# Kernel optimization log

Measured on AMD Instinct MI355X. Metric: run time of the kernel, lower is better.

Reference implementation:

```python
import jax, jax.numpy as jnp
import numpy as np

EMBED_DIM = 1024
NUM_HEADS = 16
HEAD_DIM = EMBED_DIM // NUM_HEADS


def setup_inputs() -> dict:
    key = jax.random.key(0)
    k_x, k_wqkv, k_bqkv, k_wp, k_bp = jax.random.split(key, 5)
    B, S = 4, 2048
    scale = 1.0 / np.sqrt(EMBED_DIM)
    return {
        "x": jax.random.normal(k_x, (B, S, EMBED_DIM), dtype=jnp.float32),
        # torch nn.Linear stores weight as [out_features, in_features]
        "w_qkv": jax.random.uniform(k_wqkv, (3 * EMBED_DIM, EMBED_DIM), dtype=jnp.float32, minval=-scale, maxval=scale),
        "b_qkv": jax.random.uniform(k_bqkv, (3 * EMBED_DIM,), dtype=jnp.float32, minval=-scale, maxval=scale),
        "w_proj": jax.random.uniform(k_wp, (EMBED_DIM, EMBED_DIM), dtype=jnp.float32, minval=-scale, maxval=scale),
        "b_proj": jax.random.uniform(k_bp, (EMBED_DIM,), dtype=jnp.float32, minval=-scale, maxval=scale),
    }


def reference(x, w_qkv, b_qkv, w_proj, b_proj):
    B, S, _ = x.shape
    # qkv projection: [B,S,3E]
    qkv = jnp.einsum('bse,fe->bsf', x, w_qkv) + b_qkv
    qkv = qkv.reshape(B, S, 3, NUM_HEADS, HEAD_DIM)
    qkv = jnp.transpose(qkv, (2, 0, 3, 1, 4))  # [3,B,H,S,Dh]
    q, k, v = qkv[0], qkv[1], qkv[2]
    # scaled dot-product attention (no mask, eval-mode dropout = identity)
    scores = jnp.einsum('bhqd,bhkd->bhqk', q, k) / np.sqrt(HEAD_DIM)
    attn = jax.nn.softmax(scores, axis=-1)
    out = jnp.einsum('bhqk,bhkd->bhqd', attn, v)  # [B,H,S,Dh]
    out = jnp.transpose(out, (0, 2, 1, 3)).reshape(B, S, EMBED_DIM)
    return jnp.einsum('bse,fe->bsf', out, w_proj) + b_proj
```

## Files before the change

### kernel.cpp

```cpp
#include <hip/hip_runtime.h>

#define EDIM 1024
#define NHEADS 16
#define HDIM 64
#define SEQ 2048
#define BATCH 4
#define MROWS (BATCH * SEQ)
#define NQKV (3 * EDIM)
#define QKB 2048

typedef __attribute__((ext_vector_type(4))) float f32x4;
typedef __attribute__((ext_vector_type(8))) short s16x8;
typedef __attribute__((ext_vector_type(4))) short s16x4;
typedef __attribute__((ext_vector_type(4))) unsigned int u32x4;

#define AS1 __attribute__((address_space(1)))
#define AS3 __attribute__((address_space(3)))
#define GLOAD_LDS16(g, l) __builtin_amdgcn_global_load_lds( \
    (AS1 void*)(void*)(g), (AS3 void*)(void*)(l), 16, 0, 0)

static __device__ __forceinline__ unsigned short f2bf(float f) {
  unsigned int u = __builtin_bit_cast(unsigned int, f);
  u += 0x7fffu + ((u >> 16) & 1u);
  return (unsigned short)(u >> 16);
}

static __device__ __forceinline__ float fexp2(float x) {
  float r;
  asm("v_exp_f32 %0, %1" : "=v"(r) : "v"(x));
  return r;
}

static __device__ __forceinline__ unsigned int cvtpk(float a, float b) {
  unsigned int r;
  asm("v_cvt_pk_bf16_f32 %0, %1, %2" : "=v"(r) : "v"(a), "v"(b));
  return r;
}

static __device__ __forceinline__ f32x4 mfma_bf16(s16x8 a, s16x8 b, f32x4 c) {
  return __builtin_amdgcn_mfma_f32_16x16x32_bf16(a, b, c, 0, 0, 0);
}

template <int N>
static __device__ __forceinline__ void wait_vm() {
  if constexpr (N >= 8)      asm volatile("s_waitcnt lgkmcnt(0) vmcnt(8)" ::: "memory");
  else if constexpr (N == 6) asm volatile("s_waitcnt lgkmcnt(0) vmcnt(6)" ::: "memory");
  else if constexpr (N == 4) asm volatile("s_waitcnt lgkmcnt(0) vmcnt(4)" ::: "memory");
  else if constexpr (N == 3) asm volatile("s_waitcnt lgkmcnt(0) vmcnt(3)" ::: "memory");
  else if constexpr (N == 2) asm volatile("s_waitcnt lgkmcnt(0) vmcnt(2)" ::: "memory");
  else                       asm volatile("s_waitcnt lgkmcnt(0) vmcnt(0)" ::: "memory");
}

__global__ void __launch_bounds__(256) cvt_all(const float* __restrict__ x,
                                               const float* __restrict__ wq,
                                               const float* __restrict__ wp,
                                               unsigned short* __restrict__ out) {
  const int i = blockIdx.x * 256 + threadIdx.x;
  const float* src;
  int j;
  if (i < 2097152) { src = x;  j = i; }
  else if (i < 2883584) { src = wq; j = i - 2097152; }
  else { src = wp; j = i - 2883584; }
  const float4 v = ((const float4*)src)[j];
  ushort4 o;
  o.x = f2bf(v.x); o.y = f2bf(v.y); o.z = f2bf(v.z); o.w = f2bf(v.w);
  ((ushort4*)out)[i] = o;
}

template <int MODE, int BMP, int BNP>
__global__ void __launch_bounds__(512, 2) gemm256(const unsigned short* __restrict__ Ap,
                                                  const unsigned short* __restrict__ Bp,
                                                  const float* __restrict__ bias,
                                                  void* __restrict__ Cout,
                                                  int M, int N, int K) {
  extern __shared__ unsigned short lds[];
  constexpr int ASLOT = BMP * 4096;
  constexpr int BSLOT = BNP * 4096;
  constexpr int BBASE = 4 * ASLOT;
  constexpr int L = BMP + BNP;

  const int tid = threadIdx.x;
  const int lane = tid & 63;
  const int wave = tid >> 6;
  const int wr = wave >> 2;
  const int wc = wave & 3;
  const int lr = lane & 15, kg = lane >> 4;

  const int nwg = gridDim.x;
  const int q8 = nwg >> 3;
  const int wgid = (blockIdx.x & 7) * q8 + (blockIdx.x >> 3);
  const int NBM = M >> (BMP == 2 ? 8 : 7);
  const long m0 = (long)(wgid % NBM) * (BMP * 128);
  const long n0 = (long)(wgid / NBM) * (BNP * 128);

#define STAGE(slot, kt) do {                                                   \
    _Pragma("unroll")                                                          \
    for (int i_ = 0; i_ < BMP; ++i_) {                                         \
      const int c_ = wave * BMP + i_;                \
      const int r_ = c_ * 16 + (lane >> 2);                                    \
      const int sc_ = ((lane & 3) ^ ((r_ >> 1) & 3)) * 8;                      \
      GLOAD_LDS16(Ap + (m0 + r_) * K + (kt) * 32 + sc_,                        \
                  &lds[(slot) * ASLOT + c_ * 512]);                            \
    }                                                                          \
    _Pragma("unroll")                                                          \
    for (int i_ = 0; i_ < BNP; ++i_) {                                         \
      const int c_ = wave * BNP + i_;                                          \
      const int r_ = c_ * 16 + (lane >> 2);                                    \
      const int sc_ = ((lane & 3) ^ ((r_ >> 1) & 3)) * 8;                      \
      GLOAD_LDS16(Bp + (n0 + r_) * K + (kt) * 32 + sc_,                        \
                  &lds[BBASE + (slot) * BSLOT + c_ * 512]);                    \
    }                                                                          \
  } while (0)

  f32x4 acc[BMP * 4][BNP * 2] = {};
  const int nk = K >> 5;

  STAGE(0, 0); STAGE(1, 1); STAGE(2, 2);
  wait_vm<2 * L>();
  __builtin_amdgcn_s_barrier();
  __builtin_amdgcn_sched_barrier(0);

  for (int t = 0; t < nk; ++t) {
    if (t + 3 < nk) STAGE((t + 3) & 3, t + 3);

    const unsigned short* Asl = &lds[(t & 3) * ASLOT];
    const unsigned short* Bsl = &lds[BBASE + (t & 3) * BSLOT];
    s16x8 af[BMP * 4], bf[BNP * 2];
#pragma unroll
    for (int mt = 0; mt < BMP * 4; ++mt) {
      const int r = wr * (BMP * 64) + mt * 16 + lr;
      af[mt] = *(const s16x8*)&Asl[r * 32 + ((kg * 8) ^ (((r >> 1) & 3) << 3))];
    }
#pragma unroll
    for (int nt = 0; nt < BNP * 2; ++nt) {
      const int r = wc * (BNP * 32) + nt * 16 + lr;
      bf[nt] = *(const s16x8*)&Bsl[r * 32 + ((kg * 8) ^ (((r >> 1) & 3) << 3))];
    }
    __builtin_amdgcn_s_setprio(1);
#pragma unroll
    for (int mt = 0; mt < BMP * 4; ++mt)
#pragma unroll
      for (int nt = 0; nt < BNP * 2; ++nt)
        acc[mt][nt] = mfma_bf16(af[mt], bf[nt], acc[mt][nt]);
    __builtin_amdgcn_s_setprio(0);

    if (t + 1 < nk) {
      if (t + 3 < nk)      wait_vm<2 * L>();
      else if (t + 2 < nk) wait_vm<L>();
      else                 wait_vm<0>();
      __builtin_amdgcn_s_barrier();
      __builtin_amdgcn_sched_barrier(0);
    }
  }

#pragma unroll
  for (int nt = 0; nt < BNP * 2; ++nt) {
    const long col = n0 + wc * (BNP * 32) + nt * 16 + lr;
    const float bv = (MODE == 2) ? 0.f : bias[col];
#pragma unroll
    for (int mt = 0; mt < BMP * 4; ++mt) {
#pragma unroll
      for (int r = 0; r < 4; ++r) {
        const long row = m0 + wr * (BMP * 64) + mt * 16 + kg * 4 + r;
        if (MODE == 0) {
          float v = acc[mt][nt][r] + bv;
          if (col < EDIM) v *= 0.18033688011112042f;
          ((unsigned short*)Cout)[row * QKB + col] = f2bf(v);
        } else if (MODE == 1) {
          ((float*)Cout)[row * N + col] = acc[mt][nt][r] + bv;
        } else {
          const float v = acc[mt][nt][r] + bias[row];
          ((unsigned short*)Cout)[((col >> 11) * 1024 + row) * (long)2048 +
                                  (col & 2047)] = f2bf(v);
        }
      }
    }
  }
#undef STAGE
}

__global__ void __launch_bounds__(512, 4) attn_fwd(const unsigned short* __restrict__ qk,
                                                   const unsigned short* __restrict__ vT,
                                                   unsigned short* __restrict__ attout) {
  const int L = blockIdx.x;
  const int bh = (L & 7) * 8 + (L >> 6);
  const int qt = (L >> 3) & 7;
  const int b = bh >> 4, h = bh & 15;
  const int q0 = qt * 256;
  const int tid = threadIdx.x, lane = tid & 63, wave = tid >> 6;
  const int lr = lane & 15, kg = lane >> 4;

  __shared__ unsigned short Ks[4][4096];
  __shared__ unsigned short Vs[4][4096];

  const long rowbase = (long)b * SEQ;

#define ASTAGE(slot, kv0) do {                                                  \
    const int row_ = wave * 8 + (lane >> 3);                                    \
    const int col_ = ((lane & 7) ^ (lane >> 3)) << 3;                           \
    GLOAD_LDS16(qk + (rowbase + (kv0) + row_) * QKB + EDIM + h * HDIM + col_,   \
                &Ks[slot][wave * 512]);                                         \
    GLOAD_LDS16(vT + ((long)bh * HDIM + row_) * SEQ + (kv0) + col_,             \
                &Vs[slot][wave * 512]);                                         \
  } while (0)

  s16x8 qf[2][2];
#pragma unroll
  for (int qs = 0; qs < 2; ++qs) {
    const unsigned short* qp =
        qk + (rowbase + q0 + wave * 32 + qs * 16 + lr) * QKB + h * HDIM + kg * 8;
    qf[qs][0] = *(const s16x8*)qp;
    qf[qs][1] = *(const s16x8*)(qp + 32);
  }

  f32x4 l_part[2] = {{0.f, 0.f, 0.f, 0.f}, {0.f, 0.f, 0.f, 0.f}};
  f32x4 o_acc[2][4] = {};

  ASTAGE(0, 0); ASTAGE(1, 64); ASTAGE(2, 128);
  wait_vm<4>();
  __builtin_amdgcn_s_barrier();
  __builtin_amdgcn_sched_barrier(0);

  for (int t = 0; t < 32; ++t) {
    if (t + 3 < 32) ASTAGE((t + 3) & 3, (t + 3) * 64);

    const unsigned short* Kb = Ks[t & 3];
    const unsigned short* Vb = Vs[t & 3];

    f32x4 st[2][4];
    __builtin_amdgcn_s_setprio(1);
#pragma unroll
    for (int ct = 0; ct < 4; ++ct) {
      const int rb = (ct * 16 + lr) * 128;
      const int sw = (lr & 7) << 4;
      const s16x8 k0 = *(const s16x8*)&Kb[(rb + ((kg * 16) ^ sw)) >> 1];
      const s16x8 k1 = *(const s16x8*)&Kb[(rb + ((64 + kg * 16) ^ sw)) >> 1];
#pragma unroll
      for (int qs = 0; qs < 2; ++qs) {
        f32x4 a = {};
        a = mfma_bf16(k0, qf[qs][0], a);
        a = mfma_bf16(k1, qf[qs][1], a);
        st[qs][ct] = a;
      }
    }
    __builtin_amdgcn_s_setprio(0);

    unsigned int pk[2][4][2];
#pragma unroll
    for (int qs = 0; qs < 2; ++qs) {
      f32x4 rv = {0.f, 0.f, 0.f, 0.f};
#pragma unroll
      for (int ct = 0; ct < 4; ++ct) {
        f32x4 p;
#pragma unroll
        for (int r = 0; r < 4; ++r) p[r] = fexp2(st[qs][ct][r]);
        rv += p;
        pk[qs][ct][0] = cvtpk(p[0], p[1]);
        pk[qs][ct][1] = cvtpk(p[2], p[3]);
      }
      l_part[qs] += rv;
    }

#pragma unroll
    for (int kc = 0; kc < 2; ++kc) {
      s16x8 pa[2];
#pragma unroll
      for (int qs = 0; qs < 2; ++qs) {
        u32x4 wv = {pk[qs][2 * kc][0], pk[qs][2 * kc][1],
                    pk[qs][2 * kc + 1][0], pk[qs][2 * kc + 1][1]};
        pa[qs] = __builtin_bit_cast(s16x8, wv);
      }
      __builtin_amdgcn_s_setprio(1);
#pragma unroll
      for (int dt = 0; dt < 4; ++dt) {
        const int rb = (dt * 16 + lr) * 128;
        const int c0 = (64 * kc + 8 * kg) ^ ((lr & 7) << 4);
        const s16x4 v0 = *(const s16x4*)&Vb[(rb + c0) >> 1];
        const s16x4 v1 = *(const s16x4*)&Vb[(rb + (c0 ^ 32)) >> 1];
        const s16x8 vf = __builtin_shufflevector(v0, v1, 0, 1, 2, 3, 4, 5, 6, 7);
#pragma unroll
        for (int qs = 0; qs < 2; ++qs)
          o_acc[qs][dt] = mfma_bf16(pa[qs], vf, o_acc[qs][dt]);
      }
      __builtin_amdgcn_s_setprio(0);
    }

    if (t + 1 < 32) {
      if (t + 3 < 32)      wait_vm<4>();
      else if (t + 2 < 32) wait_vm<2>();
      else                 wait_vm<0>();
      __builtin_amdgcn_s_barrier();
      __builtin_amdgcn_sched_barrier(0);
    }
  }

#pragma unroll
  for (int qs = 0; qs < 2; ++qs) {
    float rs = (l_part[qs][0] + l_part[qs][1]) + (l_part[qs][2] + l_part[qs][3]);
    rs += __shfl_xor(rs, 16, 64);
    rs += __shfl_xor(rs, 32, 64);
#pragma unroll
    for (int r = 0; r < 4; ++r) {
      const float lq = __shfl(rs, kg * 4 + r, 64);
      const float inv = 1.0f / lq;
      const long row = rowbase + q0 + wave * 32 + qs * 16 + kg * 4 + r;
#pragma unroll
      for (int dt = 0; dt < 4; ++dt)
        attout[row * EDIM + h * HDIM + dt * 16 + lr] = f2bf(o_acc[qs][dt][r] * inv);
    }
  }
#undef ASTAGE
}

extern "C" void kernel_launch(void* const* d_in, const int* in_sizes, int n_in,
                              void* d_out, int out_size, void* d_ws, size_t ws_size,
                              hipStream_t stream) {
  const float* x      = (const float*)d_in[0];
  const float* w_qkv  = (const float*)d_in[1];
  const float* b_qkv  = (const float*)d_in[2];
  const float* w_proj = (const float*)d_in[3];
  const float* b_proj = (const float*)d_in[4];

  unsigned short* xb   = (unsigned short*)d_ws;
  unsigned short* wqb  = xb   + (size_t)MROWS * EDIM;
  unsigned short* wpb  = wqb  + (size_t)NQKV * EDIM;
  unsigned short* qkb  = wpb  + (size_t)EDIM * EDIM;
  unsigned short* attb = qkb  + (size_t)MROWS * QKB;
  unsigned short* vTb  = attb + (size_t)MROWS * EDIM;

  const int sh22 = 131072;
  const int sh12 = 98304;
  const int sh21 = 98304;
  hipFuncSetAttribute((const void*)gemm256<0, 2, 2>,
                      hipFuncAttributeMaxDynamicSharedMemorySize, sh22);
  hipFuncSetAttribute((const void*)gemm256<2, 1, 2>,
                      hipFuncAttributeMaxDynamicSharedMemorySize, sh12);
  hipFuncSetAttribute((const void*)gemm256<1, 2, 1>,
                      hipFuncAttributeMaxDynamicSharedMemorySize, sh21);

  cvt_all<<<12288, 256, 0, stream>>>(x, w_qkv, w_proj, xb);

  gemm256<0, 2, 2><<<(MROWS / 256) * (QKB / 256), 512, sh22, stream>>>(
      xb, wqb, b_qkv, qkb, MROWS, QKB, EDIM);

  gemm256<2, 1, 2><<<(EDIM / 128) * (MROWS / 256), 512, sh12, stream>>>(
      wqb + (size_t)2048 * EDIM, xb, b_qkv + 2048, vTb, EDIM, MROWS, EDIM);

  attn_fwd<<<512, 512, 0, stream>>>(qkb, vTb, attb);

  gemm256<1, 2, 1><<<(MROWS / 256) * (EDIM / 128), 512, sh21, stream>>>(
      attb, wpb, b_proj, d_out, MROWS, EDIM, EDIM);
}
```

Measured before the change: 190.6 us.

## Halve attention query and KV tiles to double grid and occupancy

The attention kernel now has each block cover 128 query rows with 16 rows per wave, down from 256 and 32, and streams K/V in 32-key stages instead of 64. The grid doubles to 1024 blocks and launch bounds allow 8 blocks per SM. Half the waves now load K and the other half load V, using a new swizzle for the narrower V tile. The aim is more parallelism and latency hiding from higher occupancy. The cost is less reuse of each K/V tile across query rows, twice the loop iterations and barriers, and more global K/V traffic.

```diff
diff --git a/kernel.cpp b/kernel.cpp
--- a/kernel.cpp
+++ b/kernel.cpp
@@ -48,6 +48,7 @@
   else if constexpr (N == 4) asm volatile("s_waitcnt lgkmcnt(0) vmcnt(4)" ::: "memory");
   else if constexpr (N == 3) asm volatile("s_waitcnt lgkmcnt(0) vmcnt(3)" ::: "memory");
   else if constexpr (N == 2) asm volatile("s_waitcnt lgkmcnt(0) vmcnt(2)" ::: "memory");
+  else if constexpr (N == 1) asm volatile("s_waitcnt lgkmcnt(0) vmcnt(1)" ::: "memory");
   else                       asm volatile("s_waitcnt lgkmcnt(0) vmcnt(0)" ::: "memory");
 }
 
@@ -179,134 +180,129 @@
 #undef STAGE
 }
 
-__global__ void __launch_bounds__(512, 4) attn_fwd(const unsigned short* __restrict__ qk,
+__global__ void __launch_bounds__(512, 8) attn_fwd(const unsigned short* __restrict__ qk,
                                                    const unsigned short* __restrict__ vT,
                                                    unsigned short* __restrict__ attout) {
   const int L = blockIdx.x;
-  const int bh = (L & 7) * 8 + (L >> 6);
-  const int qt = (L >> 3) & 7;
+  const int bh = (L & 7) * 8 + (L >> 7);
+  const int qt = (L >> 3) & 15;
   const int b = bh >> 4, h = bh & 15;
-  const int q0 = qt * 256;
+  const int q0 = qt * 128;
   const int tid = threadIdx.x, lane = tid & 63, wave = tid >> 6;
   const int lr = lane & 15, kg = lane >> 4;
 
-  __shared__ unsigned short Ks[4][4096];
-  __shared__ unsigned short Vs[4][4096];
+  __shared__ unsigned short Ks[4][2048];
+  __shared__ unsigned short Vs[4][2048];
 
   const long rowbase = (long)b * SEQ;
 
 #define ASTAGE(slot, kv0) do {                                                  \
-    const int row_ = wave * 8 + (lane >> 3);                                    \
-    const int col_ = ((lane & 7) ^ (lane >> 3)) << 3;                           \
-    GLOAD_LDS16(qk + (rowbase + (kv0) + row_) * QKB + EDIM + h * HDIM + col_,   \
-                &Ks[slot][wave * 512]);                                         \
-    GLOAD_LDS16(vT + ((long)bh * HDIM + row_) * SEQ + (kv0) + col_,             \
-                &Vs[slot][wave * 512]);                                         \
+    if (wave < 4) {                                                             \
+      const int row_ = (wave & 3) * 8 + (lane >> 3);                            \
+      const int col_ = ((lane & 7) ^ (lane >> 3)) << 3;                         \
+      GLOAD_LDS16(qk + (rowbase + (kv0) + row_) * QKB + EDIM + h * HDIM + col_, \
+                  &Ks[slot][(wave & 3) * 512]);                                 \
+    } else {                                                                    \
+      const int row_ = (wave & 3) * 16 + (lane >> 2);                           \
+      const int col_ = ((lane & 3) ^ ((row_ >> 1) & 3)) << 3;                   \
+      GLOAD_LDS16(vT + ((long)bh * HDIM + row_) * SEQ + (kv0) + col_,           \
+                  &Vs[slot][(wave & 3) * 512]);                                 \
+    }                                                                           \
   } while (0)
 
-  s16x8 qf[2][2];
-#pragma unroll
-  for (int qs = 0; qs < 2; ++qs) {
+  s16x8 qf[2];
+  {
     const unsigned short* qp =
-        qk + (rowbase + q0 + wave * 32 + qs * 16 + lr) * QKB + h * HDIM + kg * 8;
-    qf[qs][0] = *(const s16x8*)qp;
-    qf[qs][1] = *(const s16x8*)(qp + 32);
-  }
-
-  f32x4 l_part[2] = {{0.f, 0.f, 0.f, 0.f}, {0.f, 0.f, 0.f, 0.f}};
-  f32x4 o_acc[2][4] = {};
-
-  ASTAGE(0, 0); ASTAGE(1, 64); ASTAGE(2, 128);
-  wait_vm<4>();
+        qk + (rowbase + q0 + wave * 16 + lr) * QKB + h * HDIM + kg * 8;
+    qf[0] = *(const s16x8*)qp;
+    qf[1] = *(const s16x8*)(qp + 32);
+  }
+
+  f32x4 l_part = {0.f, 0.f, 0.f, 0.f};
+  f32x4 o_acc[4] = {};
+
+  ASTAGE(0, 0); ASTAGE(1, 32); ASTAGE(2, 64);
+  wait_vm<2>();
   __builtin_amdgcn_s_barrier();
   __builtin_amdgcn_sched_barrier(0);
 
-  for (int t = 0; t < 32; ++t) {
-    if (t + 3 < 32) ASTAGE((t + 3) & 3, (t + 3) * 64);
+  for (int t = 0; t < 64; ++t) {
+    if (t + 3 < 64) ASTAGE((t + 3) & 3, (t + 3) * 32);
 
     const unsigned short* Kb = Ks[t & 3];
     const unsigned short* Vb = Vs[t & 3];
 
-    f32x4 st[2][4];
+    f32x4 st[2];
     __builtin_amdgcn_s_setprio(1);
 #pragma unroll
-    for (int ct = 0; ct < 4; ++ct) {
+    for (int ct = 0; ct < 2; ++ct) {
       const int rb = (ct * 16 + lr) * 128;
       const int sw = (lr & 7) << 4;
       const s16x8 k0 = *(const s16x8*)&Kb[(rb + ((kg * 16) ^ sw)) >> 1];
       const s16x8 k1 = *(const s16x8*)&Kb[(rb + ((64 + kg * 16) ^ sw)) >> 1];
-#pragma unroll
-      for (int qs = 0; qs < 2; ++qs) {
-        f32x4 a = {};
-        a = mfma_bf16(k0, qf[qs][0], a);
-        a = mfma_bf16(k1, qf[qs][1], a);
-        st[qs][ct] = a;
+      f32x4 a = {};
+      a = mfma_bf16(k0, qf[0], a);
+      a = mfma_bf16(k1, qf[1], a);
+      st[ct] = a;
+    }
+    __builtin_amdgcn_s_setprio(0);
+
+    unsigned int pk[2][2];
+    {
+      f32x4 rv = {0.f, 0.f, 0.f, 0.f};
+#pragma unroll
+      for (int ct = 0; ct < 2; ++ct) {
+        f32x4 p;
+#pragma unroll
+        for (int r = 0; r < 4; ++r) p[r] = fexp2(st[ct][r]);
+        rv += p;
+        pk[ct][0] = cvtpk(p[0], p[1]);
+        pk[ct][1] = cvtpk(p[2], p[3]);
       }
-    }
-    __builtin_amdgcn_s_setprio(0);
-
-    unsigned int pk[2][4][2];
-#pragma unroll
-    for (int qs = 0; qs < 2; ++qs) {
-      f32x4 rv = {0.f, 0.f, 0.f, 0.f};
-#pragma unroll
-      for (int ct = 0; ct < 4; ++ct) {
-        f32x4 p;
-#pragma unroll
-        for (int r = 0; r < 4; ++r) p[r] = fexp2(st[qs][ct][r]);
-        rv += p;
-        pk[qs][ct][0] = cvtpk(p[0], p[1]);
-        pk[qs][ct][1] = cvtpk(p[2], p[3]);
-      }
-      l_part[qs] += rv;
-    }
-
-#pragma unroll
-    for (int kc = 0; kc < 2; ++kc) {
-      s16x8 pa[2];
-#pragma unroll
-      for (int qs = 0; qs < 2; ++qs) {
-        u32x4 wv = {pk[qs][2 * kc][0], pk[qs][2 * kc][1],
-                    pk[qs][2 * kc + 1][0], pk[qs][2 * kc + 1][1]};
-        pa[qs] = __builtin_bit_cast(s16x8, wv);
-      }
+      l_part += rv;
+    }
+
+    {
+      u32x4 wv = {pk[0][0], pk[0][1], pk[1][0], pk[1][1]};
+      const s16x8 pa = __builtin_bit_cast(s16x8, wv);
       __builtin_amdgcn_s_setprio(1);
 #pragma unroll
       for (int dt = 0; dt < 4; ++dt) {
-        const int rb = (dt * 16 + lr) * 128;
-        const int c0 = (64 * kc + 8 * kg) ^ ((lr & 7) << 4);
-        const s16x4 v0 = *(const s16x4*)&Vb[(rb + c0) >> 1];
-        const s16x4 v1 = *(const s16x4*)&Vb[(rb + (c0 ^ 32)) >> 1];
+        const int d = dt * 16 + lr;
+        const int rb = d * 64;
+        const int xs = ((d >> 1) & 3) << 4;
+        const int lo = (kg & 1) << 3;
+        const int b0 = (((kg >> 1) << 4) ^ xs) + lo;
+        const int b1 = ((32 + ((kg >> 1) << 4)) ^ xs) + lo;
+        const s16x4 v0 = *(const s16x4*)&Vb[(rb + b0) >> 1];
+        const s16x4 v1 = *(const s16x4*)&Vb[(rb + b1) >> 1];
         const s16x8 vf = __builtin_shufflevector(v0, v1, 0, 1, 2, 3, 4, 5, 6, 7);
-#pragma unroll
-        for (int qs = 0; qs < 2; ++qs)
-          o_acc[qs][dt] = mfma_bf16(pa[qs], vf, o_acc[qs][dt]);
+        o_acc[dt] = mfma_bf16(pa, vf, o_acc[dt]);
       }
       __builtin_amdgcn_s_setprio(0);
     }
 
-    if (t + 1 < 32) {
-      if (t + 3 < 32)      wait_vm<4>();
-      else if (t + 2 < 32) wait_vm<2>();
+    if (t + 1 < 64) {
+      if (t + 3 < 64)      wait_vm<2>();
+      else if (t + 2 < 64) wait_vm<1>();
       else                 wait_vm<0>();
       __builtin_amdgcn_s_barrier();
       __builtin_amdgcn_sched_barrier(0);
     }
   }
 
-#pragma unroll
-  for (int qs = 0; qs < 2; ++qs) {
-    float rs = (l_part[qs][0] + l_part[qs][1]) + (l_part[qs][2] + l_part[qs][3]);
+  {
+    float rs = (l_part[0] + l_part[1]) + (l_part[2] + l_part[3]);
     rs += __shfl_xor(rs, 16, 64);
     rs += __shfl_xor(rs, 32, 64);
 #pragma unroll
     for (int r = 0; r < 4; ++r) {
       const float lq = __shfl(rs, kg * 4 + r, 64);
       const float inv = 1.0f / lq;
-      const long row = rowbase + q0 + wave * 32 + qs * 16 + kg * 4 + r;
+      const long row = rowbase + q0 + wave * 16 + kg * 4 + r;
 #pragma unroll
       for (int dt = 0; dt < 4; ++dt)
-        attout[row * EDIM + h * HDIM + dt * 16 + lr] = f2bf(o_acc[qs][dt][r] * inv);
+        attout[row * EDIM + h * HDIM + dt * 16 + lr] = f2bf(o_acc[dt][r] * inv);
     }
   }
 #undef ASTAGE
@@ -346,7 +342,7 @@
   gemm256<2, 1, 2><<<(EDIM / 128) * (MROWS / 256), 512, sh12, stream>>>(
       wqb + (size_t)2048 * EDIM, xb, b_qkv + 2048, vTb, EDIM, MROWS, EDIM);
 
-  attn_fwd<<<512, 512, 0, stream>>>(qkb, vTb, attb);
+  attn_fwd<<<1024, 512, 0, stream>>>(qkb, vTb, attb);
 
   gemm256<1, 2, 1><<<(MROWS / 256) * (EDIM / 128), 512, sh21, stream>>>(
       attb, wpb, b_proj, d_out, MROWS, EDIM, EDIM);
```

Measured after the change: 218.9 us. +14.8%, slower.

## Restructure GEMM into 8-phase ping-pong schedule with 64-wide K tiles

Applied to the files above, without the earlier changes.

Replaces the 4-slot, K=32 multistage GEMM loop with a double-buffered K=64 scheme. Each iteration is split into eight phases that interleave LDS fragment loads, half-tile global-to-LDS stages and quarter-tile MFMA blocks, with barriers between phases. The aim is to overlap memory traffic with matrix-core work at finer granularity and halve the number of K iterations. It changes the LDS swizzle to 64-element rows and adds many more barriers, which risks extra synchronization overhead or hazards.

```diff
diff --git a/kernel.cpp b/kernel.cpp
--- a/kernel.cpp
+++ b/kernel.cpp
@@ -68,16 +68,15 @@
 }
 
 template <int MODE, int BMP, int BNP>
-__global__ void __launch_bounds__(512, 2) gemm256(const unsigned short* __restrict__ Ap,
-                                                  const unsigned short* __restrict__ Bp,
-                                                  const float* __restrict__ bias,
-                                                  void* __restrict__ Cout,
-                                                  int M, int N, int K) {
+__global__ void __launch_bounds__(512, 2) gemm8p(const unsigned short* __restrict__ Ap,
+                                                 const unsigned short* __restrict__ Bp,
+                                                 const float* __restrict__ bias,
+                                                 void* __restrict__ Cout,
+                                                 int M, int N, int K) {
   extern __shared__ unsigned short lds[];
-  constexpr int ASLOT = BMP * 4096;
-  constexpr int BSLOT = BNP * 4096;
-  constexpr int BBASE = 4 * ASLOT;
-  constexpr int L = BMP + BNP;
+  constexpr int AHALF = BMP * 4096;
+  constexpr int BHALF = BNP * 4096;
+  constexpr int BBASE = 4 * AHALF;
 
   const int tid = threadIdx.x;
   const int lane = tid & 63;
@@ -93,64 +92,108 @@
   const long m0 = (long)(wgid % NBM) * (BMP * 128);
   const long n0 = (long)(wgid / NBM) * (BNP * 128);
 
-#define STAGE(slot, kt) do {                                                   \
-    _Pragma("unroll")                                                          \
-    for (int i_ = 0; i_ < BMP; ++i_) {                                         \
-      const int c_ = wave * BMP + i_;                \
-      const int r_ = c_ * 16 + (lane >> 2);                                    \
-      const int sc_ = ((lane & 3) ^ ((r_ >> 1) & 3)) * 8;                      \
-      GLOAD_LDS16(Ap + (m0 + r_) * K + (kt) * 32 + sc_,                        \
-                  &lds[(slot) * ASLOT + c_ * 512]);                            \
-    }                                                                          \
-    _Pragma("unroll")                                                          \
-    for (int i_ = 0; i_ < BNP; ++i_) {                                         \
-      const int c_ = wave * BNP + i_;                                          \
-      const int r_ = c_ * 16 + (lane >> 2);                                    \
-      const int sc_ = ((lane & 3) ^ ((r_ >> 1) & 3)) * 8;                      \
-      GLOAD_LDS16(Bp + (n0 + r_) * K + (kt) * 32 + sc_,                        \
-                  &lds[BBASE + (slot) * BSLOT + c_ * 512]);                    \
-    }                                                                          \
-  } while (0)
+#define SA(buf, half, kt) do {                                                  \
+    _Pragma("unroll")                                                           \
+    for (int i_ = 0; i_ < BMP; ++i_) {                                          \
+      const int rh_ = i_ * 64 + wave * 8 + (lane >> 3);                         \
+      const int ce_ = ((lane & 7) ^ (lane >> 3)) * 8;                           \
+      GLOAD_LDS16(Ap + (m0 + (half) * (BMP * 64) + rh_) * K + (kt) * 64 + ce_,  \
+                  &lds[(buf) * 2 * AHALF + (half) * AHALF + i_ * 4096 + wave * 512]); \
+    } } while (0)
+#define SB(buf, half, kt) do {                                                  \
+    _Pragma("unroll")                                                           \
+    for (int i_ = 0; i_ < BNP; ++i_) {                                          \
+      const int rh_ = i_ * 64 + wave * 8 + (lane >> 3);                         \
+      const int ce_ = ((lane & 7) ^ (lane >> 3)) * 8;                           \
+      GLOAD_LDS16(Bp + (n0 + (half) * (BNP * 64) + rh_) * K + (kt) * 64 + ce_,  \
+                  &lds[BBASE + (buf) * 2 * BHALF + (half) * BHALF + i_ * 4096 + wave * 512]); \
+    } } while (0)
+
+#define PH_ENTER() do { __builtin_amdgcn_s_barrier();                           \
+    asm volatile("s_waitcnt lgkmcnt(0)" ::: "memory");                          \
+    __builtin_amdgcn_sched_barrier(0); } while (0)
+#define PH_EXIT() __builtin_amdgcn_s_barrier()
+#define PH_EXIT_VM() do { wait_vm<2 * BNP>();                                   \
+    __builtin_amdgcn_sched_barrier(0);                                          \
+    __builtin_amdgcn_s_barrier(); } while (0)
+#define PH_EXIT_VM0() do { wait_vm<0>();                                        \
+    __builtin_amdgcn_sched_barrier(0);                                          \
+    __builtin_amdgcn_s_barrier(); } while (0)
 
   f32x4 acc[BMP * 4][BNP * 2] = {};
-  const int nk = K >> 5;
-
-  STAGE(0, 0); STAGE(1, 1); STAGE(2, 2);
-  wait_vm<2 * L>();
+  s16x8 af[2 * BMP][2], bf0[BNP][2], bf1[BNP][2];
+
+  auto LA = [&](int buf, int qm) {
+#pragma unroll
+    for (int m = 0; m < 2 * BMP; ++m) {
+      const int rh = qm * (BMP * 32) + m * 16 + lr;
+      const int ro = (buf * 2 + wr) * AHALF + rh * 64;
+#pragma unroll
+      for (int ks = 0; ks < 2; ++ks)
+        af[m][ks] = *(const s16x8*)
+            &lds[ro + (((ks * 64 + kg * 16) ^ ((rh & 7) << 4)) >> 1)];
+    }
+  };
+  auto LB = [&](int buf, int qn, s16x8 (&bf)[BNP][2]) {
+#pragma unroll
+    for (int n = 0; n < BNP; ++n) {
+      const int rh = (wc & 1) * (BNP * 32) + qn * (BNP * 16) + n * 16 + lr;
+      const int ro = BBASE + (buf * 2 + (wc >> 1)) * BHALF + rh * 64;
+#pragma unroll
+      for (int ks = 0; ks < 2; ++ks)
+        bf[n][ks] = *(const s16x8*)
+            &lds[ro + (((ks * 64 + kg * 16) ^ ((rh & 7) << 4)) >> 1)];
+    }
+  };
+  auto MM = [&](int qm, int qn, s16x8 (&bf)[BNP][2]) {
+    __builtin_amdgcn_s_setprio(1);
+#pragma unroll
+    for (int m = 0; m < 2 * BMP; ++m)
+#pragma unroll
+      for (int n = 0; n < BNP; ++n)
+#pragma unroll
+        for (int ks = 0; ks < 2; ++ks)
+          acc[qm * 2 * BMP + m][qn * BNP + n] =
+              mfma_bf16(af[m][ks], bf[n][ks], acc[qm * 2 * BMP + m][qn * BNP + n]);
+    __builtin_amdgcn_s_setprio(0);
+  };
+
+  const int nk = K >> 6;
+  const int nit = nk >> 1;
+
+  SB(0, 0, 0); SB(0, 1, 0);
+  SA(0, 0, 0); SA(0, 1, 0);
+  SB(1, 0, 1); SB(1, 1, 1);
+  wait_vm<2 * BNP>();
+  __builtin_amdgcn_sched_barrier(0);
   __builtin_amdgcn_s_barrier();
   __builtin_amdgcn_sched_barrier(0);
 
-  for (int t = 0; t < nk; ++t) {
-    if (t + 3 < nk) STAGE((t + 3) & 3, t + 3);
-
-    const unsigned short* Asl = &lds[(t & 3) * ASLOT];
-    const unsigned short* Bsl = &lds[BBASE + (t & 3) * BSLOT];
-    s16x8 af[BMP * 4], bf[BNP * 2];
-#pragma unroll
-    for (int mt = 0; mt < BMP * 4; ++mt) {
-      const int r = wr * (BMP * 64) + mt * 16 + lr;
-      af[mt] = *(const s16x8*)&Asl[r * 32 + ((kg * 8) ^ (((r >> 1) & 3) << 3))];
-    }
-#pragma unroll
-    for (int nt = 0; nt < BNP * 2; ++nt) {
-      const int r = wc * (BNP * 32) + nt * 16 + lr;
-      bf[nt] = *(const s16x8*)&Bsl[r * 32 + ((kg * 8) ^ (((r >> 1) & 3) << 3))];
-    }
-    __builtin_amdgcn_s_setprio(1);
-#pragma unroll
-    for (int mt = 0; mt < BMP * 4; ++mt)
-#pragma unroll
-      for (int nt = 0; nt < BNP * 2; ++nt)
-        acc[mt][nt] = mfma_bf16(af[mt], bf[nt], acc[mt][nt]);
-    __builtin_amdgcn_s_setprio(0);
-
-    if (t + 1 < nk) {
-      if (t + 3 < nk)      wait_vm<2 * L>();
-      else if (t + 2 < nk) wait_vm<L>();
-      else                 wait_vm<0>();
-      __builtin_amdgcn_s_barrier();
-      __builtin_amdgcn_sched_barrier(0);
-    }
+  for (int it = 0; it < nit; ++it) {
+    const int ta = 2 * it, tb = 2 * it + 1;
+    LA(0, 0); LB(0, 0, bf0);
+    SA(1, 0, tb);
+    PH_ENTER(); MM(0, 0, bf0); PH_EXIT();
+    LB(0, 1, bf1);
+    SA(1, 1, tb);
+    PH_ENTER(); MM(0, 1, bf1); PH_EXIT();
+    LA(0, 1);
+    if (ta + 2 < nk) SB(0, 0, ta + 2);
+    PH_ENTER(); MM(1, 0, bf0); PH_EXIT();
+    if (ta + 2 < nk) SB(0, 1, ta + 2);
+    PH_ENTER(); MM(1, 1, bf1);
+    if (it + 1 < nit) { PH_EXIT_VM(); } else { PH_EXIT_VM0(); }
+    LA(1, 0); LB(1, 0, bf0);
+    if (ta + 2 < nk) SA(0, 0, ta + 2);
+    PH_ENTER(); MM(0, 0, bf0); PH_EXIT();
+    LB(1, 1, bf1);
+    if (ta + 2 < nk) SA(0, 1, ta + 2);
+    PH_ENTER(); MM(0, 1, bf1); PH_EXIT();
+    LA(1, 1);
+    if (tb + 2 < nk) SB(1, 0, tb + 2);
+    PH_ENTER(); MM(1, 0, bf0); PH_EXIT();
+    if (tb + 2 < nk) SB(1, 1, tb + 2);
+    PH_ENTER(); MM(1, 1, bf1); PH_EXIT_VM();
   }
 
 #pragma unroll
@@ -176,7 +219,12 @@
       }
     }
   }
-#undef STAGE
+#undef SA
+#undef SB
+#undef PH_ENTER
+#undef PH_EXIT
+#undef PH_EXIT_VM
+#undef PH_EXIT_VM0
 }
 
 __global__ void __launch_bounds__(512, 4) attn_fwd(const unsigned short* __restrict__ qk,
@@ -331,23 +379,23 @@
   const int sh22 = 131072;
   const int sh12 = 98304;
   const int sh21 = 98304;
-  hipFuncSetAttribute((const void*)gemm256<0, 2, 2>,
+  hipFuncSetAttribute((const void*)gemm8p<0, 2, 2>,
                       hipFuncAttributeMaxDynamicSharedMemorySize, sh22);
-  hipFuncSetAttribute((const void*)gemm256<2, 1, 2>,
+  hipFuncSetAttribute((const void*)gemm8p<2, 1, 2>,
                       hipFuncAttributeMaxDynamicSharedMemorySize, sh12);
-  hipFuncSetAttribute((const void*)gemm256<1, 2, 1>,
+  hipFuncSetAttribute((const void*)gemm8p<1, 2, 1>,
                       hipFuncAttributeMaxDynamicSharedMemorySize, sh21);
 
   cvt_all<<<12288, 256, 0, stream>>>(x, w_qkv, w_proj, xb);
 
-  gemm256<0, 2, 2><<<(MROWS / 256) * (QKB / 256), 512, sh22, stream>>>(
+  gemm8p<0, 2, 2><<<(MROWS / 256) * (QKB / 256), 512, sh22, stream>>>(
       xb, wqb, b_qkv, qkb, MROWS, QKB, EDIM);
 
-  gemm256<2, 1, 2><<<(EDIM / 128) * (MROWS / 256), 512, sh12, stream>>>(
+  gemm8p<2, 1, 2><<<(EDIM / 128) * (MROWS / 256), 512, sh12, stream>>>(
       wqb + (size_t)2048 * EDIM, xb, b_qkv + 2048, vTb, EDIM, MROWS, EDIM);
 
   attn_fwd<<<512, 512, 0, stream>>>(qkb, vTb, attb);
 
-  gemm256<1, 2, 1><<<(MROWS / 256) * (EDIM / 128), 512, sh21, stream>>>(
+  gemm8p<1, 2, 1><<<(MROWS / 256) * (EDIM / 128), 512, sh21, stream>>>(
       attb, wpb, b_proj, d_out, MROWS, EDIM, EDIM);
 }
```

Measured after the change: 187.4 us, median of 2. About the same (-1.7%).
